# Kernel tuning notes

Measured on AMD Instinct MI355X. Metric: run time of the kernel, lower is better.

The kernel has to match this reference:

```python
import jax, jax.numpy as jnp
import numpy as np

LAYERS, UNITS, B, T = 3, 1024, 128, 256


def setup_inputs() -> dict:
    key = jax.random.key(0)
    k1, k2, k3, k4, k5 = jax.random.split(key, 5)
    scale = 0.03  # keep gate pre-activations in a sane range
    return {
        "input_seq": jax.random.normal(k1, (B, T, UNITS), dtype=jnp.float32),
        "initial_states": jax.random.normal(k2, (B, UNITS, LAYERS), dtype=jnp.float32),
        "W": jax.random.normal(k3, (LAYERS, UNITS, 3 * UNITS), dtype=jnp.float32) * scale,
        "U": jax.random.normal(k4, (LAYERS, UNITS, 3 * UNITS), dtype=jnp.float32) * scale,
        "b": jax.random.normal(k5, (LAYERS, 2, 3 * UNITS), dtype=jnp.float32) * scale,
    }


def _gru_layer(x, h0, Wl, Ul, bl):
    """Keras GRU (reset_after=True), inference mode. x: [B,T,F], h0: [B,U]."""
    u = h0.shape[-1]
    # Precompute input projections for all timesteps: [B,T,3U] -> scan over T.
    xw = jnp.einsum("btf,fg->btg", x, Wl) + bl[0]
    xw_t = jnp.swapaxes(xw, 0, 1)  # [T,B,3U]

    def step(h, xw_step):
        hu = h @ Ul + bl[1]  # [B,3U]
        xz, xr, xh = xw_step[:, :u], xw_step[:, u:2 * u], xw_step[:, 2 * u:]
        hz, hr, hh = hu[:, :u], hu[:, u:2 * u], hu[:, 2 * u:]
        z = jax.nn.sigmoid(xz + hz)
        r = jax.nn.sigmoid(xr + hr)
        hhat = jnp.tanh(xh + r * hh)
        h_new = z * h + (1.0 - z) * hhat
        return h_new, h_new

    h_last, ys = jax.lax.scan(step, h0, xw_t)
    return jnp.swapaxes(ys, 0, 1), h_last  # [B,T,U], [B,U]


def reference(input_seq, initial_states, W, U, b):
    x = input_seq
    states = []
    for i in range(LAYERS):
        x, h = _gru_layer(x, initial_states[:, :, i], W[i], U[i], b[i])
        states.append(h)
    return x, jnp.stack(states, axis=-1)  # [B,T,U], [B,U,L]
```

## Files before the change

kernel.cpp:

```cpp
#include <hip/hip_runtime.h>
#include <cstdint>
#include <cstddef>


#define UNITS 1024
#define U3 3072
#define BATCH 128
#define TSTEPS 256

typedef _Float16 h16;
typedef __attribute__((ext_vector_type(8))) _Float16 h16x8;
typedef __attribute__((ext_vector_type(4))) _Float16 h16x4;
typedef __attribute__((ext_vector_type(4))) float f32x4;
typedef __attribute__((ext_vector_type(4))) unsigned int u32x4;

#define GAS __attribute__((address_space(1)))
#define LAS __attribute__((address_space(3)))
#define ASYNC16(g, l) __builtin_amdgcn_global_load_lds((const GAS unsigned int*)(g), (LAS unsigned int*)(l), 16, 0, 0)

__device__ __forceinline__ float sigmf(float x) { return 1.0f / (1.0f + __expf(-x)); }
__device__ __forceinline__ float tanhf_fast(float x) { return 2.0f / (1.0f + __expf(-2.0f * x)) - 1.0f; }

__global__ void k_cvt_x(const float* __restrict__ x, h16* __restrict__ xo) {
  const int m = blockIdx.x;
  const int t = m >> 7, b = m & 127;
  const int u = threadIdx.x << 2;
  const float4 v = *(const float4*)(x + (size_t)((b << 8) + t) * UNITS + u);
  h16x4 o; o[0] = (h16)v.x; o[1] = (h16)v.y; o[2] = (h16)v.z; o[3] = (h16)v.w;
  *(h16x4*)(xo + (size_t)m * UNITS + u) = o;
}

__global__ void k_trans(const float* __restrict__ src, h16* __restrict__ dst) {
  __shared__ float sT[32][33];
  const int l = blockIdx.z;
  const int n0 = blockIdx.x << 5, k0 = blockIdx.y << 5;
  const int tx = threadIdx.x, ty = threadIdx.y;
  const float* s = src + (size_t)l * UNITS * U3;
  h16* d = dst + (size_t)l * U3 * UNITS;
#pragma unroll
  for (int r = 0; r < 4; ++r)
    sT[ty + r * 8][tx] = s[(size_t)(k0 + ty + r * 8) * U3 + n0 + tx];
  __syncthreads();
#pragma unroll
  for (int r = 0; r < 4; ++r)
    d[(size_t)(n0 + ty + r * 8) * UNITS + k0 + tx] = (h16)sT[tx][ty + r * 8];
}

__global__ void k_cvt_h(const float* __restrict__ init, h16* __restrict__ h0) {
  const int idx = blockIdx.x * 256 + threadIdx.x;
  const int l = idx >> 17, r = idx & 131071;
  h0[idx] = (h16)init[(size_t)r * 3 + l];
}

__global__ void k_zero(int* __restrict__ p, int n) {
  const int i = blockIdx.x * 256 + threadIdx.x;
  if (i < n) p[i] = 0;
}

__global__ __launch_bounds__(256) void k_gemm_xw(
    const h16* __restrict__ A, const h16* __restrict__ Bt,
    const float* __restrict__ bias, h16* __restrict__ C) {
  __shared__ __align__(16) h16 sA[128 * 32];
  __shared__ __align__(16) h16 sB[128 * 32];
  const int tid = threadIdx.x;
  const int lane = tid & 63, wave = tid >> 6;
  const int wm = (wave & 1) << 6, wn = (wave >> 1) << 6;
  const int m0 = blockIdx.x << 7;
  const int n0 = blockIdx.y << 7;
  const int crow = tid >> 2, ck = (tid & 3) << 3;
  const int fm = lane & 15, fq = lane >> 4;
  f32x4 acc[4][4] = {};
  for (int k0 = 0; k0 < 1024; k0 += 32) {
    ASYNC16(A + (size_t)(m0 + crow) * 1024 + k0 + ck,      sA + wave * 512);
    ASYNC16(A + (size_t)(m0 + 64 + crow) * 1024 + k0 + ck, sA + 2048 + wave * 512);
    ASYNC16(Bt + (size_t)(n0 + crow) * 1024 + k0 + ck,      sB + wave * 512);
    ASYNC16(Bt + (size_t)(n0 + 64 + crow) * 1024 + k0 + ck, sB + 2048 + wave * 512);
    __syncthreads();
    h16x8 af[4], bfv[4];
#pragma unroll
    for (int i = 0; i < 4; ++i)
      af[i] = *(const h16x8*)(sA + (wm + i * 16 + fm) * 32 + fq * 8);
#pragma unroll
    for (int j = 0; j < 4; ++j)
      bfv[j] = *(const h16x8*)(sB + (wn + j * 16 + fm) * 32 + fq * 8);
#pragma unroll
    for (int i = 0; i < 4; ++i)
#pragma unroll
      for (int j = 0; j < 4; ++j)
        acc[i][j] = __builtin_amdgcn_mfma_f32_16x16x32_f16(af[i], bfv[j], acc[i][j], 0, 0, 0);
    __syncthreads();
  }
#pragma unroll
  for (int j = 0; j < 4; ++j) {
    const int col = n0 + wn + j * 16 + fm;
    const float bv = bias[col];
#pragma unroll
    for (int i = 0; i < 4; ++i) {
      const int row = m0 + wm + i * 16 + fq * 4;
#pragma unroll
      for (int r = 0; r < 4; ++r)
        C[(size_t)(row + r) * U3 + col] = (h16)(acc[i][j][r] + bv);
    }
  }
}

__global__ __launch_bounds__(128, 1) void k_rec(
    const h16* __restrict__ Ut,
    const float* __restrict__ b1,
    const h16* __restrict__ xw,
    const h16* __restrict__ h0l,
    h16* __restrict__ P0,
    h16* __restrict__ P1,
    h16* __restrict__ y16,
    float* __restrict__ yf,
    float* __restrict__ st,
    int* __restrict__ flags,
    const int l) {
  __shared__ __align__(16) h16 sU[49152];
  const int tid = threadIdx.x;
  const int lane = tid & 63, w = tid >> 6;
  const int b = blockIdx.x;
  const int c = b & 63, rg = b >> 6;
  const int c0 = c << 4;
  const int fm = lane & 15, fq = lane >> 4;

#pragma unroll
  for (int kk = 0; kk < 32; ++kk) {
#pragma unroll
    for (int g = 0; g < 3; ++g) {
      const int i = kk * 3 + g;
      if ((i & 1) == w)
        ASYNC16(Ut + (size_t)((g << 10) + c0 + fm) * 1024 + (kk << 5) + (fq << 3),
                sU + (size_t)i * 512);
    }
  }
  const int col = c0 + fm;
  const float bz = b1[col], br = b1[1024 + col], bh = b1[2048 + col];
  const int r0 = (rg << 5) + (w << 4);
  const int rowA = r0 + fm;
  const int rQ = r0 + (fq << 2);
  const int* fpoll = flags + (rg << 7) + ((lane & 31) << 2);
  int* fpost = flags + (rg << 7) + (c << 1) + w;
  __syncthreads();

  for (int t = 0; t < TSTEPS; ++t) {
    if (t > 0) {
      const int target = (l << 8) + t;
      u32x4 f;
      do {
        asm volatile("global_load_dwordx4 %0, %1, off sc0 sc1\n\ts_waitcnt vmcnt(0)"
                     : "=v"(f) : "v"(fpoll) : "memory");
      } while (!__all((int)f[0] >= target && (int)f[1] >= target &&
                      (int)f[2] >= target && (int)f[3] >= target));
    }
    const h16* hin = (t == 0) ? h0l : ((t & 1) ? P0 : P1);
    h16* hout = (t & 1) ? P1 : P0;

    u32x4 raw[32];
    const h16* Ab = hin + (size_t)rowA * 1024 + (fq << 3);
#pragma unroll
    for (int kk = 0; kk < 32; ++kk)
      asm volatile("global_load_dwordx4 %0, %1, off offset:%2 sc0 sc1"
                   : "=v"(raw[kk]) : "v"(Ab), "n"(kk * 64));
    unsigned int hpu[4];
    const h16* hqa = hin + (size_t)rQ * 1024 + col;
    const h16* hqb = hqa + 2048;
    asm volatile("global_load_ushort %0, %1, off sc0 sc1"             : "=v"(hpu[0]) : "v"(hqa));
    asm volatile("global_load_ushort %0, %1, off offset:2048 sc0 sc1" : "=v"(hpu[1]) : "v"(hqa));
    asm volatile("global_load_ushort %0, %1, off sc0 sc1"             : "=v"(hpu[2]) : "v"(hqb));
    asm volatile("global_load_ushort %0, %1, off offset:2048 sc0 sc1" : "=v"(hpu[3]) : "v"(hqb));
    unsigned int xwb[12];
    {
      const h16* xq = xw + (size_t)(t * 128 + rQ) * U3 + col;
#pragma unroll
      for (int r = 0; r < 4; ++r) {
        const h16* xa = xq + (size_t)r * U3;
        const h16* xb2 = xa + 2048;
        asm volatile("global_load_ushort %0, %1, off"             : "=v"(xwb[r * 3 + 0]) : "v"(xa));
        asm volatile("global_load_ushort %0, %1, off offset:2048" : "=v"(xwb[r * 3 + 1]) : "v"(xa));
        asm volatile("global_load_ushort %0, %1, off"             : "=v"(xwb[r * 3 + 2]) : "v"(xb2));
      }
    }

    f32x4 a0 = {}, a1 = {}, a2 = {};
#pragma unroll
    for (int half = 0; half < 2; ++half) {
      if (half == 0) asm volatile("s_waitcnt vmcnt(32)" ::: "memory");
      else           asm volatile("s_waitcnt vmcnt(16)" ::: "memory");
      __builtin_amdgcn_sched_barrier(0);
#pragma unroll
      for (int kk = half * 16; kk < half * 16 + 16; ++kk) {
        union { u32x4 u; h16x8 h; } ac; ac.u = raw[kk];
        const h16* bb = sU + (size_t)(kk * 3) * 512 + (lane << 3);
        const h16x8 vz = *(const h16x8*)(bb);
        const h16x8 vr = *(const h16x8*)(bb + 512);
        const h16x8 vh = *(const h16x8*)(bb + 1024);
        a0 = __builtin_amdgcn_mfma_f32_16x16x32_f16(ac.h, vz, a0, 0, 0, 0);
        a1 = __builtin_amdgcn_mfma_f32_16x16x32_f16(ac.h, vr, a1, 0, 0, 0);
        a2 = __builtin_amdgcn_mfma_f32_16x16x32_f16(ac.h, vh, a2, 0, 0, 0);
      }
    }
    asm volatile("s_waitcnt vmcnt(0)" ::: "memory");
    __builtin_amdgcn_sched_barrier(0);

    h16* so = hout + (size_t)rQ * 1024 + col;
    float hn[4];
#pragma unroll
    for (int r = 0; r < 4; ++r) {
      union { unsigned short s; h16 h; } cv;
      cv.s = (unsigned short)hpu[r];       const float hp = (float)cv.h;
      cv.s = (unsigned short)xwb[r * 3 + 0]; const float xz = (float)cv.h;
      cv.s = (unsigned short)xwb[r * 3 + 1]; const float xr = (float)cv.h;
      cv.s = (unsigned short)xwb[r * 3 + 2]; const float xh = (float)cv.h;
      const float z   = sigmf(xz + a0[r] + bz);
      const float rgt = sigmf(xr + a1[r] + br);
      const float hh  = tanhf_fast(xh + rgt * (a2[r] + bh));
      hn[r] = z * hp + (1.0f - z) * hh;
      union { unsigned short s; h16 h; } ov; ov.h = (h16)hn[r];
      const unsigned int ob = ov.s;
      if (r == 0) asm volatile("global_store_short %0, %1, off sc0 sc1"             :: "v"(so), "v"(ob) : "memory");
      if (r == 1) asm volatile("global_store_short %0, %1, off offset:2048 sc0 sc1" :: "v"(so), "v"(ob) : "memory");
      if (r == 2) asm volatile("global_store_short %0, %1, off sc0 sc1"             :: "v"(so + 2048), "v"(ob) : "memory");
      if (r == 3) asm volatile("global_store_short %0, %1, off offset:2048 sc0 sc1" :: "v"(so + 2048), "v"(ob) : "memory");
    }
    asm volatile("s_waitcnt vmcnt(0)" ::: "memory");
    if (lane == 0) {
      const int fv = (l << 8) + t + 1;
      asm volatile("global_store_dword %0, %1, off sc0 sc1" :: "v"(fpost), "v"(fv) : "memory");
    }
#pragma unroll
    for (int r = 0; r < 4; ++r) {
      const int row = rQ + r;
      if (y16) y16[(size_t)(t * 128 + row) * 1024 + col] = (h16)hn[r];
      if (yf)  yf[(size_t)(row * 256 + t) * 1024 + col] = hn[r];
      if (t == 255) st[(size_t)(row * 1024 + col) * 3] = hn[r];
    }
  }
}

extern "C" void kernel_launch(void* const* d_in, const int* in_sizes, int n_in,
                              void* d_out, int out_size, void* d_ws, size_t ws_size,
                              hipStream_t stream) {
  const float* x_in  = (const float*)d_in[0];
  const float* h0_in = (const float*)d_in[1];
  const float* W     = (const float*)d_in[2];
  const float* U     = (const float*)d_in[3];
  const float* bias  = (const float*)d_in[4];
  float* out = (float*)d_out;

  char* ws = (char*)d_ws;
  h16* x16 = (h16*)(ws);
  h16* xw  = (h16*)(ws + 67108864);
  h16* Wt  = (h16*)(ws + 268435456);
  h16* Ut  = (h16*)(ws + 287309824);
  h16* h0b = (h16*)(ws + 306184192);
  h16* P0  = (h16*)(ws + 306970624);

  h16* P1A    = (h16*)((char*)d_out + 134217728 - 262144);
  int* flagsA = (int*)((char*)d_out + 134217728 - 262144 - 16384);
  h16* P1B    = (h16*)ws;
  int* flags2 = (int*)(ws + 262144);

  k_cvt_x<<<TSTEPS * BATCH, 256, 0, stream>>>(x_in, x16);
  k_trans<<<dim3(96, 32, 3), dim3(32, 8), 0, stream>>>(W, Wt);
  k_trans<<<dim3(96, 32, 3), dim3(32, 8), 0, stream>>>(U, Ut);
  k_cvt_h<<<1536, 256, 0, stream>>>(h0_in, h0b);
  k_zero<<<16, 256, 0, stream>>>(flagsA, 4096);

  for (int l = 0; l < 3; ++l) {
    const float* b0 = bias + (size_t)l * 6144;
    const float* b1 = bias + (size_t)l * 6144 + 3072;
    k_gemm_xw<<<dim3(256, 24), 256, 0, stream>>>(x16, Wt + (size_t)l * U3 * UNITS, b0, xw);
    if (l == 2) k_zero<<<16, 256, 0, stream>>>(flags2, 4096);
    h16* P1    = (l < 2) ? P1A : P1B;
    int* flags = (l < 2) ? flagsA : flags2;
    h16* y16p  = (l < 2) ? x16 : nullptr;
    float* yfp = (l == 2) ? out : nullptr;
    float* stp = out + 33554432 + l;
    k_rec<<<256, 128, 0, stream>>>(Ut + (size_t)l * U3 * UNITS, b1, xw,
                                   h0b + (size_t)l * BATCH * UNITS,
                                   P0, P1, y16p, yfp, stp, flags, l);
  }
}
```

Before: 5.994 ms.

## Replace per-wave flag polling with atomic step counters and cache half of U in registers

The grid barrier changes from polling 128 per-wave flags with a vector load and wave-wide vote to a single per-row-group counter per timestep. Each wave atomically increments it and pollers spin on one dword until it reaches the expected count, which accumulates across layers. The first half of the recurrent weight fragments is also preloaded from LDS into registers once, and the MFMA loop is split into four chunks with finer vmcnt waits. The aims are a cheaper barrier and fewer LDS reads per step. The cost is higher register pressure and atomic contention on one counter per group.

```diff
diff --git a/kernel.cpp b/kernel.cpp
--- a/kernel.cpp
+++ b/kernel.cpp
@@ -114,8 +114,8 @@
     h16* __restrict__ y16,
     float* __restrict__ yf,
     float* __restrict__ st,
-    int* __restrict__ flags,
-    const int l) {
+    int* __restrict__ cnt,
+    const int tgt) {
   __shared__ __align__(16) h16 sU[49152];
   const int tid = threadIdx.x;
   const int lane = tid & 63, w = tid >> 6;
@@ -139,19 +139,26 @@
   const int r0 = (rg << 5) + (w << 4);
   const int rowA = r0 + fm;
   const int rQ = r0 + (fq << 2);
-  const int* fpoll = flags + (rg << 7) + ((lane & 31) << 2);
-  int* fpost = flags + (rg << 7) + (c << 1) + w;
+  int* cbase = cnt + (rg << 8);
   __syncthreads();
+
+  h16x8 Bz[16], Br[16], Bh[16];
+#pragma unroll
+  for (int kk = 0; kk < 16; ++kk) {
+    const h16* bb = sU + (size_t)(kk * 3) * 512 + (lane << 3);
+    Bz[kk] = *(const h16x8*)(bb);
+    Br[kk] = *(const h16x8*)(bb + 512);
+    Bh[kk] = *(const h16x8*)(bb + 1024);
+  }
 
   for (int t = 0; t < TSTEPS; ++t) {
     if (t > 0) {
-      const int target = (l << 8) + t;
-      u32x4 f;
+      const int* cp = cbase + t - 1;
+      int f;
       do {
-        asm volatile("global_load_dwordx4 %0, %1, off sc0 sc1\n\ts_waitcnt vmcnt(0)"
-                     : "=v"(f) : "v"(fpoll) : "memory");
-      } while (!__all((int)f[0] >= target && (int)f[1] >= target &&
-                      (int)f[2] >= target && (int)f[3] >= target));
+        asm volatile("global_load_dword %0, %1, off sc0 sc1\n\ts_waitcnt vmcnt(0)"
+                     : "=v"(f) : "v"(cp) : "memory");
+      } while (f < tgt);
     }
     const h16* hin = (t == 0) ? h0l : ((t & 1) ? P0 : P1);
     h16* hout = (t & 1) ? P1 : P0;
@@ -184,20 +191,28 @@
 
     f32x4 a0 = {}, a1 = {}, a2 = {};
 #pragma unroll
-    for (int half = 0; half < 2; ++half) {
-      if (half == 0) asm volatile("s_waitcnt vmcnt(32)" ::: "memory");
-      else           asm volatile("s_waitcnt vmcnt(16)" ::: "memory");
+    for (int ch = 0; ch < 4; ++ch) {
+      if (ch == 0) asm volatile("s_waitcnt vmcnt(40)" ::: "memory");
+      if (ch == 1) asm volatile("s_waitcnt vmcnt(32)" ::: "memory");
+      if (ch == 2) asm volatile("s_waitcnt vmcnt(24)" ::: "memory");
+      if (ch == 3) asm volatile("s_waitcnt vmcnt(16)" ::: "memory");
       __builtin_amdgcn_sched_barrier(0);
 #pragma unroll
-      for (int kk = half * 16; kk < half * 16 + 16; ++kk) {
+      for (int kk = ch * 8; kk < ch * 8 + 8; ++kk) {
         union { u32x4 u; h16x8 h; } ac; ac.u = raw[kk];
-        const h16* bb = sU + (size_t)(kk * 3) * 512 + (lane << 3);
-        const h16x8 vz = *(const h16x8*)(bb);
-        const h16x8 vr = *(const h16x8*)(bb + 512);
-        const h16x8 vh = *(const h16x8*)(bb + 1024);
-        a0 = __builtin_amdgcn_mfma_f32_16x16x32_f16(ac.h, vz, a0, 0, 0, 0);
-        a1 = __builtin_amdgcn_mfma_f32_16x16x32_f16(ac.h, vr, a1, 0, 0, 0);
-        a2 = __builtin_amdgcn_mfma_f32_16x16x32_f16(ac.h, vh, a2, 0, 0, 0);
+        if (kk < 16) {
+          a0 = __builtin_amdgcn_mfma_f32_16x16x32_f16(ac.h, Bz[kk], a0, 0, 0, 0);
+          a1 = __builtin_amdgcn_mfma_f32_16x16x32_f16(ac.h, Br[kk], a1, 0, 0, 0);
+          a2 = __builtin_amdgcn_mfma_f32_16x16x32_f16(ac.h, Bh[kk], a2, 0, 0, 0);
+        } else {
+          const h16* bb = sU + (size_t)(kk * 3) * 512 + (lane << 3);
+          const h16x8 vz = *(const h16x8*)(bb);
+          const h16x8 vr = *(const h16x8*)(bb + 512);
+          const h16x8 vh = *(const h16x8*)(bb + 1024);
+          a0 = __builtin_amdgcn_mfma_f32_16x16x32_f16(ac.h, vz, a0, 0, 0, 0);
+          a1 = __builtin_amdgcn_mfma_f32_16x16x32_f16(ac.h, vr, a1, 0, 0, 0);
+          a2 = __builtin_amdgcn_mfma_f32_16x16x32_f16(ac.h, vh, a2, 0, 0, 0);
+        }
       }
     }
     asm volatile("s_waitcnt vmcnt(0)" ::: "memory");
@@ -208,7 +223,7 @@
 #pragma unroll
     for (int r = 0; r < 4; ++r) {
       union { unsigned short s; h16 h; } cv;
-      cv.s = (unsigned short)hpu[r];       const float hp = (float)cv.h;
+      cv.s = (unsigned short)hpu[r];         const float hp = (float)cv.h;
       cv.s = (unsigned short)xwb[r * 3 + 0]; const float xz = (float)cv.h;
       cv.s = (unsigned short)xwb[r * 3 + 1]; const float xr = (float)cv.h;
       cv.s = (unsigned short)xwb[r * 3 + 2]; const float xh = (float)cv.h;
@@ -224,10 +239,9 @@
       if (r == 3) asm volatile("global_store_short %0, %1, off offset:2048 sc0 sc1" :: "v"(so + 2048), "v"(ob) : "memory");
     }
     asm volatile("s_waitcnt vmcnt(0)" ::: "memory");
-    if (lane == 0) {
-      const int fv = (l << 8) + t + 1;
-      asm volatile("global_store_dword %0, %1, off sc0 sc1" :: "v"(fpost), "v"(fv) : "memory");
-    }
+    if (lane == 0)
+      (void)__hip_atomic_fetch_add(cbase + t, 1, __ATOMIC_RELAXED,
+                                   __HIP_MEMORY_SCOPE_AGENT);
 #pragma unroll
     for (int r = 0; r < 4; ++r) {
       const int row = rQ + r;
@@ -256,29 +270,30 @@
   h16* h0b = (h16*)(ws + 306184192);
   h16* P0  = (h16*)(ws + 306970624);
 
-  h16* P1A    = (h16*)((char*)d_out + 134217728 - 262144);
-  int* flagsA = (int*)((char*)d_out + 134217728 - 262144 - 16384);
-  h16* P1B    = (h16*)ws;
-  int* flags2 = (int*)(ws + 262144);
+  h16* P1A   = (h16*)((char*)d_out + 134217728 - 262144);
+  int* cntA  = (int*)((char*)d_out + 134217728 - 262144 - 16384);
+  h16* P1B   = (h16*)ws;
+  int* cntB  = (int*)(ws + 262144);
 
   k_cvt_x<<<TSTEPS * BATCH, 256, 0, stream>>>(x_in, x16);
   k_trans<<<dim3(96, 32, 3), dim3(32, 8), 0, stream>>>(W, Wt);
   k_trans<<<dim3(96, 32, 3), dim3(32, 8), 0, stream>>>(U, Ut);
   k_cvt_h<<<1536, 256, 0, stream>>>(h0_in, h0b);
-  k_zero<<<16, 256, 0, stream>>>(flagsA, 4096);
+  k_zero<<<4, 256, 0, stream>>>(cntA, 1024);
 
   for (int l = 0; l < 3; ++l) {
     const float* b0 = bias + (size_t)l * 6144;
     const float* b1 = bias + (size_t)l * 6144 + 3072;
     k_gemm_xw<<<dim3(256, 24), 256, 0, stream>>>(x16, Wt + (size_t)l * U3 * UNITS, b0, xw);
-    if (l == 2) k_zero<<<16, 256, 0, stream>>>(flags2, 4096);
-    h16* P1    = (l < 2) ? P1A : P1B;
-    int* flags = (l < 2) ? flagsA : flags2;
+    if (l == 2) k_zero<<<4, 256, 0, stream>>>(cntB, 1024);
+    h16* P1   = (l < 2) ? P1A : P1B;
+    int* cnt  = (l < 2) ? cntA : cntB;
+    const int tgt = (l < 2) ? (l + 1) * 128 : 128;
     h16* y16p  = (l < 2) ? x16 : nullptr;
     float* yfp = (l == 2) ? out : nullptr;
     float* stp = out + 33554432 + l;
     k_rec<<<256, 128, 0, stream>>>(Ut + (size_t)l * U3 * UNITS, b1, xw,
                                    h0b + (size_t)l * BATCH * UNITS,
-                                   P0, P1, y16p, yfp, stp, flags, l);
-  }
-}
+                                   P0, P1, y16p, yfp, stp, cnt, tgt);
+  }
+}
```

Measured after the change: 6.064 ms. About the same (+1.2%).
